# Performance work log

Hardware: AMD Instinct MI355X
Metric: run time of the kernel (lower is better)

The kernel has to match this reference:

```python
import jax, jax.numpy as jnp
import numpy as np

NUM_KERNELS = 5


def setup_inputs() -> dict:
    key = jax.random.key(0)
    k1, k2 = jax.random.split(key)
    B, D = 4096, 256
    return {
        "s_feat": jax.random.normal(k1, (B, D), dtype=jnp.float32),
        "t_feat": jax.random.normal(k2, (B, D), dtype=jnp.float32),
    }


def _pairwise_sq_dists(feats):
    # Gram-matrix form of sum((x_i - x_j)**2, axis=-1); same math as the
    # broadcasted (x - y)**2 sum, without the [N, N, D] intermediate.
    sq = jnp.sum(feats * feats, axis=-1)  # [N]
    d = sq[:, None] + sq[None, :] - 2.0 * (feats @ feats.T)  # [N, N]
    return jnp.maximum(d, 0.0)


def reference(s_feat, t_feat):
    batch = s_feat.shape[0]
    feats = jnp.concatenate((s_feat, t_feat), axis=0)  # [2B, D]
    distances = _pairwise_sq_dists(feats)  # [2B, 2B]

    # Median-heuristic-style bandwidth (detached in original).
    n = 2 * batch
    bandwidth = float(n * n - n) / jnp.sum(jax.lax.stop_gradient(distances))
    bandwidth = bandwidth / (2 ** (NUM_KERNELS // 2))
    gammas = [bandwidth * (2 ** i) for i in range(NUM_KERNELS)]

    # Multi-gamma Gaussian kernel average (fixed small loop over kernels).
    kern = sum(jnp.exp(-distances * g) for g in gammas) / NUM_KERNELS

    s2s = kern[:batch, :batch]
    t2t = kern[batch:, batch:]
    s2t = kern[:batch, batch:]
    disc = jnp.mean(s2s + t2t - 2.0 * s2t)
    return disc
```

## Files before the change

kernel.cpp:

```cpp
#include <hip/hip_runtime.h>
#include <stdint.h>
#include <math.h>

#define BATCH 4096
#define NT    8192
#define FD    256
#define TILE  128
#define BK    32
#define NUMK  5
#define NTRI  2080
#define PBLK  1024

typedef __attribute__((ext_vector_type(8))) short bf16x8;
typedef __attribute__((ext_vector_type(4))) float f32x4;

static const size_t WS_FB    = 0;
static const size_t WS_SQ    = (size_t)NT * FD * 2;
static const size_t WS_PCOL  = WS_SQ + (size_t)NT * 4;
static const size_t WS_WSUM  = WS_PCOL + (size_t)PBLK * 256 * 4;
static const size_t WS_GAMMA = WS_WSUM + (size_t)PBLK * 4;

__device__ __forceinline__ unsigned short f2bf_rne(float x) {
    unsigned u = __float_as_uint(x);
    unsigned r = (u + 0x7fffu + ((u >> 16) & 1u)) >> 16;
    return (unsigned short)r;
}

__device__ __forceinline__ void async_copy16(void* lds, const void* g) {
    __builtin_amdgcn_global_load_lds(
        (__attribute__((address_space(1))) void*)(void*)(const_cast<void*>(g)),
        (__attribute__((address_space(3))) void*)lds, 16, 0, 0);
}

__global__ void mmd_prep(const float* __restrict__ s_feat,
                         const float* __restrict__ t_feat,
                         unsigned short* __restrict__ fb,
                         float* __restrict__ sq,
                         float* __restrict__ pcol,
                         float* __restrict__ wsum) {
    __shared__ float cp[4][FD];
    __shared__ float rw[4];
    const int w    = threadIdx.x >> 6;
    const int lane = threadIdx.x & 63;
    float c0 = 0.f, c1 = 0.f, c2 = 0.f, c3 = 0.f;
    float wtot = 0.f;
#pragma unroll
    for (int t = 0; t < 2; ++t) {
        int row = blockIdx.x * 8 + w * 2 + t;
        const float* src = (row < BATCH) ? (s_feat + (size_t)row * FD)
                                         : (t_feat + (size_t)(row - BATCH) * FD);
        float4 v = ((const float4*)src)[lane];
        unsigned int u01 = (unsigned)f2bf_rne(v.x) | ((unsigned)f2bf_rne(v.y) << 16);
        unsigned int u23 = (unsigned)f2bf_rne(v.z) | ((unsigned)f2bf_rne(v.w) << 16);
        ((uint2*)(fb + (size_t)row * FD))[lane] = make_uint2(u01, u23);
        float ss = v.x * v.x + v.y * v.y + v.z * v.z + v.w * v.w;
        for (int off = 32; off; off >>= 1) ss += __shfl_down(ss, off);
        if (lane == 0) { sq[row] = ss; wtot += ss; }
        c0 += v.x; c1 += v.y; c2 += v.z; c3 += v.w;
    }
    cp[w][4 * lane + 0] = c0;
    cp[w][4 * lane + 1] = c1;
    cp[w][4 * lane + 2] = c2;
    cp[w][4 * lane + 3] = c3;
    if (lane == 0) rw[w] = wtot;
    __syncthreads();
    int t = threadIdx.x;
    pcol[(size_t)blockIdx.x * 256 + t] = cp[0][t] + cp[1][t] + cp[2][t] + cp[3][t];
    if (t == 0) wsum[blockIdx.x] = rw[0] + rw[1] + rw[2] + rw[3];
}

__global__ void mmd_gamma(const float* __restrict__ pcol,
                          const float* __restrict__ wsum,
                          float* __restrict__ gamma,
                          float* __restrict__ out) {
    __shared__ float gcol[4][256];
    __shared__ float redc[4], redw[16];
    const int tid  = threadIdx.x;
    const int c    = tid & 255, s = tid >> 8;
    const int lane = tid & 63;
    float a0 = 0.f, a1 = 0.f, a2 = 0.f, a3 = 0.f;
#pragma unroll 4
    for (int k = 0; k < 256; k += 4) {
        a0 += pcol[(size_t)(s * 256 + k + 0) * 256 + c];
        a1 += pcol[(size_t)(s * 256 + k + 1) * 256 + c];
        a2 += pcol[(size_t)(s * 256 + k + 2) * 256 + c];
        a3 += pcol[(size_t)(s * 256 + k + 3) * 256 + c];
    }
    gcol[s][c] = (a0 + a1) + (a2 + a3);
    float wv = wsum[tid];
    for (int off = 32; off; off >>= 1) wv += __shfl_down(wv, off);
    if (lane == 0) redw[tid >> 6] = wv;
    __syncthreads();
    if (tid < 256) {
        float colv = gcol[0][c] + gcol[1][c] + gcol[2][c] + gcol[3][c];
        float cv2 = colv * colv;
        for (int off = 32; off; off >>= 1) cv2 += __shfl_down(cv2, off);
        if (lane == 0) redc[tid >> 6] = cv2;
    }
    __syncthreads();
    if (tid == 0) {
        float s2 = (redc[0] + redc[1]) + (redc[2] + redc[3]);
        float ssq = 0.f;
#pragma unroll
        for (int i = 0; i < 16; ++i) ssq += redw[i];
        float sumd = 2.0f * (float)NT * ssq - 2.0f * s2;
        float n2n  = (float)((long long)NT * NT - NT);
        gamma[0]   = 0.25f * (n2n / sumd);
        out[0]     = 0.f;
    }
}

__global__ __launch_bounds__(256, 2) void mmd_main(
    const unsigned short* __restrict__ fb,
    const float* __restrict__ sq,
    const float* __restrict__ gamma,
    float* __restrict__ out) {
    const int bid = blockIdx.x;
    const int swz = (bid & 7) * (NTRI / 8) + (bid >> 3);
    int r = (int)((sqrtf(8.0f * (float)swz + 1.0f) - 1.0f) * 0.5f);
    while ((r + 1) * (r + 2) / 2 <= swz) ++r;
    while (r * (r + 1) / 2 > swz) --r;
    const int bi = swz - r * (r + 1) / 2;
    const int bj = r;

    __shared__ __align__(16) unsigned short a_t[4][2][64 * BK];
    __shared__ __align__(16) unsigned short b_t[4][2][64 * BK];
    __shared__ float sqa[TILE], sqb[TILE];
    __shared__ float red[4];

    const int tid  = threadIdx.x;
    const int w    = tid >> 6, lane = tid & 63;
    const int wm   = w >> 1, wn = w & 1;
    const int quad = lane >> 4, m16 = lane & 15;
    const int lrow16 = lane >> 2;
    const int pslot  = lane & 3;

    const size_t rowA0 = (size_t)bi * TILE + wm * 64;
    const size_t rowB0 = (size_t)bj * TILE + wn * 64;

    float sqv = 0.f;
    if (tid < TILE) sqv = sq[(size_t)bi * TILE + tid];
    else            sqv = sq[(size_t)bj * TILE + (tid - TILE)];
    const float g0 = gamma[0];

#define STAGE_W(buf, k0_) do {                                                 \
        _Pragma("unroll")                                                      \
        for (int q = 0; q < 4; ++q) {                                          \
            int rr_ = q * 16 + lrow16;                    \
            int gc_ = pslot ^ ((rr_ >> 1) & 3);                                \
            async_copy16(&a_t[w][buf][(q * 16) * BK],                          \
                         fb + (rowA0 + rr_) * FD + (k0_) + gc_ * 8);           \
        }                                                                      \
        _Pragma("unroll")                                                      \
        for (int q = 0; q < 4; ++q) {                                          \
            int rr_ = q * 16 + lrow16;                                         \
            int gc_ = pslot ^ ((rr_ >> 1) & 3);                                \
            async_copy16(&b_t[w][buf][(q * 16) * BK],                          \
                         fb + (rowB0 + rr_) * FD + (k0_) + gc_ * 8);           \
        }                                                                      \
    } while (0)

    STAGE_W(0, 0);
    STAGE_W(1, BK);

    if (tid < TILE) sqa[tid] = sqv;
    else            sqb[tid - TILE] = sqv;

    const f32x4 fzero = {0.f, 0.f, 0.f, 0.f};
    f32x4 acc[4][4];
#pragma unroll
    for (int a = 0; a < 4; ++a)
#pragma unroll
        for (int b = 0; b < 4; ++b) acc[a][b] = fzero;

#pragma unroll
    for (int st = 0; st < 8; ++st) {
        const int cur = st & 1;
        if (st == 7) asm volatile("s_waitcnt vmcnt(0)" ::: "memory");
        else         asm volatile("s_waitcnt vmcnt(8)" ::: "memory");
        __builtin_amdgcn_sched_barrier(0);

        bf16x8 af[4], bf[4];
#pragma unroll
        for (int tm = 0; tm < 4; ++tm) {
            int ra = tm * 16 + m16;
            int p = quad ^ ((ra >> 1) & 3);
            af[tm] = *(const bf16x8*)&a_t[w][cur][ra * BK + p * 8];
        }
#pragma unroll
        for (int tn = 0; tn < 4; ++tn) {
            int rb = tn * 16 + m16;
            int p = quad ^ ((rb >> 1) & 3);
            bf[tn] = *(const bf16x8*)&b_t[w][cur][rb * BK + p * 8];
        }
        asm volatile("s_waitcnt lgkmcnt(0)" ::: "memory");
        __builtin_amdgcn_sched_barrier(0);
        if (st < 6) STAGE_W(cur, (st + 2) * BK);
        __builtin_amdgcn_sched_barrier(0);

        __builtin_amdgcn_s_setprio(1);
#pragma unroll
        for (int tm = 0; tm < 4; ++tm)
#pragma unroll
            for (int tn = 0; tn < 4; ++tn)
                acc[tm][tn] = __builtin_amdgcn_mfma_f32_16x16x32_bf16(
                    af[tm], bf[tn], acc[tm][tn], 0, 0, 0);
        __builtin_amdgcn_s_setprio(0);
    }

    __syncthreads();

    float ls[4] = {0.f, 0.f, 0.f, 0.f};
#pragma unroll
    for (int tm = 0; tm < 4; ++tm) {
        const int i0 = wm * 64 + tm * 16 + quad * 4;
        float sqi[4] = {sqa[i0 + 0], sqa[i0 + 1], sqa[i0 + 2], sqa[i0 + 3]};
#pragma unroll
        for (int tn = 0; tn < 4; ++tn) {
            const int j = wn * 64 + tn * 16 + m16;
            const float sqj = sqb[j];
#pragma unroll
            for (int rr = 0; rr < 4; ++rr) {
                float d = fmaf(-2.f, acc[tm][tn][rr], sqi[rr] + sqj);
                d = fmaxf(d, 0.f);
                float e1 = __expf(-d * g0);
                float e2 = e1 * e1, e4 = e2 * e2, e8 = e4 * e4, e16 = e8 * e8;
                ls[rr] += e1 + e2 + e4 + e8 + e16;
            }
        }
    }
    float lsum = (ls[0] + ls[1]) + (ls[2] + ls[3]);
    for (int off = 32; off; off >>= 1) lsum += __shfl_down(lsum, off);
    if (lane == 0) red[w] = lsum;
    __syncthreads();
    if (tid == 0) {
        float wgt;
        if (bi == bj) wgt = 1.f;
        else wgt = ((bi < 32) == (bj < 32)) ? 2.f : -2.f;
        float scale = wgt * (1.f / NUMK) * (1.f / 16777216.f);
        atomicAdd(out, (red[0] + red[1] + red[2] + red[3]) * scale);
    }
}

extern "C" void kernel_launch(void* const* d_in, const int* in_sizes, int n_in,
                              void* d_out, int out_size, void* d_ws, size_t ws_size,
                              hipStream_t stream) {
    const float* s_feat = (const float*)d_in[0];
    const float* t_feat = (const float*)d_in[1];
    char* ws = (char*)d_ws;
    unsigned short* fb = (unsigned short*)(ws + WS_FB);
    float* sq    = (float*)(ws + WS_SQ);
    float* pcol  = (float*)(ws + WS_PCOL);
    float* wsum  = (float*)(ws + WS_WSUM);
    float* gamma = (float*)(ws + WS_GAMMA);
    float* out   = (float*)d_out;

    mmd_prep<<<PBLK, 256, 0, stream>>>(s_feat, t_feat, fb, sq, pcol, wsum);
    mmd_gamma<<<1, 1024, 0, stream>>>(pcol, wsum, gamma, out);
    mmd_main<<<NTRI, 256, 0, stream>>>(fb, sq, gamma, out);
}
```

Before: 117.4 us.

## Load MFMA operands directly from global into registers with triple buffering

Removes the LDS staging path (async global-to-LDS copies, swizzled LDS reads, waitcnt choreography). Each wave now loads its bf16 operand fragments straight from global memory into registers, prefetching three K-steps ahead in a rotating register buffer. The aim is to cut LDS traffic and synchronization, since each wave already uses its own private tiles. In exchange, register pressure rises (24 bf16x8 operand vectors) and the global loads are strided per row and rely on the compiler's waitcnt placement, which may expose memory latency.

Measured after the change: 144.1 us. 22.7% more time.

```diff
diff --git a/kernel.cpp b/kernel.cpp
--- a/kernel.cpp
+++ b/kernel.cpp
@@ -6,7 +6,6 @@
 #define NT    8192
 #define FD    256
 #define TILE  128
-#define BK    32
 #define NUMK  5
 #define NTRI  2080
 #define PBLK  1024
@@ -24,12 +23,6 @@
     unsigned u = __float_as_uint(x);
     unsigned r = (u + 0x7fffu + ((u >> 16) & 1u)) >> 16;
     return (unsigned short)r;
-}
-
-__device__ __forceinline__ void async_copy16(void* lds, const void* g) {
-    __builtin_amdgcn_global_load_lds(
-        (__attribute__((address_space(1))) void*)(void*)(const_cast<void*>(g)),
-        (__attribute__((address_space(3))) void*)lds, 16, 0, 0);
 }
 
 __global__ void mmd_prep(const float* __restrict__ s_feat,
@@ -123,8 +116,6 @@
     const int bi = swz - r * (r + 1) / 2;
     const int bj = r;
 
-    __shared__ __align__(16) unsigned short a_t[4][2][64 * BK];
-    __shared__ __align__(16) unsigned short b_t[4][2][64 * BK];
     __shared__ float sqa[TILE], sqb[TILE];
     __shared__ float red[4];
 
@@ -132,37 +123,28 @@
     const int w    = tid >> 6, lane = tid & 63;
     const int wm   = w >> 1, wn = w & 1;
     const int quad = lane >> 4, m16 = lane & 15;
-    const int lrow16 = lane >> 2;
-    const int pslot  = lane & 3;
-
-    const size_t rowA0 = (size_t)bi * TILE + wm * 64;
-    const size_t rowB0 = (size_t)bj * TILE + wn * 64;
+
+    const unsigned short* pa =
+        fb + ((size_t)bi * TILE + wm * 64 + m16) * FD + quad * 8;
+    const unsigned short* pb =
+        fb + ((size_t)bj * TILE + wn * 64 + m16) * FD + quad * 8;
+
+    bf16x8 af[3][4], bf[3][4];
+#pragma unroll
+    for (int s = 0; s < 3; ++s) {
+#pragma unroll
+        for (int tm = 0; tm < 4; ++tm)
+            af[s][tm] = *(const bf16x8*)(pa + tm * 16 * FD + s * 32);
+#pragma unroll
+        for (int tn = 0; tn < 4; ++tn)
+            bf[s][tn] = *(const bf16x8*)(pb + tn * 16 * FD + s * 32);
+    }
+    __builtin_amdgcn_sched_barrier(0);
 
     float sqv = 0.f;
     if (tid < TILE) sqv = sq[(size_t)bi * TILE + tid];
     else            sqv = sq[(size_t)bj * TILE + (tid - TILE)];
     const float g0 = gamma[0];
-
-#define STAGE_W(buf, k0_) do {                                                 \
-        _Pragma("unroll")                                                      \
-        for (int q = 0; q < 4; ++q) {                                          \
-            int rr_ = q * 16 + lrow16;                    \
-            int gc_ = pslot ^ ((rr_ >> 1) & 3);                                \
-            async_copy16(&a_t[w][buf][(q * 16) * BK],                          \
-                         fb + (rowA0 + rr_) * FD + (k0_) + gc_ * 8);           \
-        }                                                                      \
-        _Pragma("unroll")                                                      \
-        for (int q = 0; q < 4; ++q) {                                          \
-            int rr_ = q * 16 + lrow16;                                         \
-            int gc_ = pslot ^ ((rr_ >> 1) & 3);                                \
-            async_copy16(&b_t[w][buf][(q * 16) * BK],                          \
-                         fb + (rowB0 + rr_) * FD + (k0_) + gc_ * 8);           \
-        }                                                                      \
-    } while (0)
-
-    STAGE_W(0, 0);
-    STAGE_W(1, BK);
-
     if (tid < TILE) sqa[tid] = sqv;
     else            sqb[tid - TILE] = sqv;
 
@@ -175,28 +157,7 @@
 
 #pragma unroll
     for (int st = 0; st < 8; ++st) {
-        const int cur = st & 1;
-        if (st == 7) asm volatile("s_waitcnt vmcnt(0)" ::: "memory");
-        else         asm volatile("s_waitcnt vmcnt(8)" ::: "memory");
-        __builtin_amdgcn_sched_barrier(0);
-
-        bf16x8 af[4], bf[4];
-#pragma unroll
-        for (int tm = 0; tm < 4; ++tm) {
-            int ra = tm * 16 + m16;
-            int p = quad ^ ((ra >> 1) & 3);
-            af[tm] = *(const bf16x8*)&a_t[w][cur][ra * BK + p * 8];
-        }
-#pragma unroll
-        for (int tn = 0; tn < 4; ++tn) {
-            int rb = tn * 16 + m16;
-            int p = quad ^ ((rb >> 1) & 3);
-            bf[tn] = *(const bf16x8*)&b_t[w][cur][rb * BK + p * 8];
-        }
-        asm volatile("s_waitcnt lgkmcnt(0)" ::: "memory");
-        __builtin_amdgcn_sched_barrier(0);
-        if (st < 6) STAGE_W(cur, (st + 2) * BK);
-        __builtin_amdgcn_sched_barrier(0);
+        const int cur = st % 3;
 
         __builtin_amdgcn_s_setprio(1);
 #pragma unroll
@@ -204,8 +165,19 @@
 #pragma unroll
             for (int tn = 0; tn < 4; ++tn)
                 acc[tm][tn] = __builtin_amdgcn_mfma_f32_16x16x32_bf16(
-                    af[tm], bf[tn], acc[tm][tn], 0, 0, 0);
+                    af[cur][tm], bf[cur][tn], acc[tm][tn], 0, 0, 0);
         __builtin_amdgcn_s_setprio(0);
+        __builtin_amdgcn_sched_barrier(0);
+
+        if (st <= 4) {
+#pragma unroll
+            for (int tm = 0; tm < 4; ++tm)
+                af[cur][tm] = *(const bf16x8*)(pa + tm * 16 * FD + (st + 3) * 32);
+#pragma unroll
+            for (int tn = 0; tn < 4; ++tn)
+                bf[cur][tn] = *(const bf16x8*)(pb + tn * 16 * FD + (st + 3) * 32);
+        }
+        __builtin_amdgcn_sched_barrier(0);
     }
 
     __syncthreads();
```
